# Optimization experiments

Measured on AMD Instinct MI355X. Metric: run time of the kernel, lower is better.

## Reference

```python
import jax, jax.numpy as jnp
import numpy as np
from jax.ops import segment_sum, segment_max

N_NODES = 100000
N_EDGES = 1600000
IN_CH = 128
HIDDEN = 128
OUT_CH = 64
HEADS1 = 8


def _lin_params(key, din, dout, scale):
    kw, kb = jax.random.split(key)
    W = jax.random.normal(kw, (din, dout), jnp.float32) * scale
    b = jax.random.normal(kb, (dout,), jnp.float32) * 0.01
    return W, b


def setup_inputs() -> dict:
    key = jax.random.key(0)
    ks = jax.random.split(key, 10)
    x = jax.random.normal(ks[0], (N_NODES, IN_CH), jnp.float32)
    edge_index = jax.random.randint(ks[1], (2, N_EDGES), 0, N_NODES, jnp.int32)
    s1 = 1.0 / np.sqrt(IN_CH)
    Wq1, bq1 = _lin_params(ks[2], IN_CH, HIDDEN, s1)
    Wk1, bk1 = _lin_params(ks[3], IN_CH, HIDDEN, s1)
    Wv1, bv1 = _lin_params(ks[4], IN_CH, HIDDEN, s1)
    Ws1, bs1 = _lin_params(ks[5], IN_CH, HIDDEN, s1)
    s2 = 1.0 / np.sqrt(HIDDEN)
    Wq2, bq2 = _lin_params(ks[6], HIDDEN, OUT_CH, s2)
    Wk2, bk2 = _lin_params(ks[7], HIDDEN, OUT_CH, s2)
    Wv2, bv2 = _lin_params(ks[8], HIDDEN, OUT_CH, s2)
    Ws2, bs2 = _lin_params(ks[9], HIDDEN, OUT_CH, s2)
    return dict(x=x, edge_index=edge_index,
                Wq1=Wq1, bq1=bq1, Wk1=Wk1, bk1=bk1, Wv1=Wv1, bv1=bv1, Ws1=Ws1, bs1=bs1,
                Wq2=Wq2, bq2=bq2, Wk2=Wk2, bk2=bk2, Wv2=Wv2, bv2=bv2, Ws2=Ws2, bs2=bs2)


def transformer_conv(x, src, dst, Wq, bq, Wk, bk, Wv, bv, Ws, bs, heads, concat):
    # x: [N, Din]; src/dst: [E]; per-head dim C = Dout_total // heads
    N = x.shape[0]
    C = Wq.shape[1] // heads
    q = (x @ Wq + bq).reshape(N, heads, C)
    k = (x @ Wk + bk).reshape(N, heads, C)
    v = (x @ Wv + bv).reshape(N, heads, C)
    # edge-wise gather + dot-product attention logits: [E, H]
    alpha = jnp.einsum('ehc,ehc->eh', q[dst], k[src]) / np.sqrt(C)
    # softmax over incoming edges of each dst node (stable via segment max)
    m = segment_max(alpha, dst, num_segments=N)  # [N, H]
    ex = jnp.exp(alpha - jax.lax.stop_gradient(m)[dst])
    denom = segment_sum(ex, dst, num_segments=N)  # [N, H]
    alpha_n = ex / denom[dst]  # [E, H]
    out = segment_sum(v[src] * alpha_n[:, :, None], dst, num_segments=N)  # [N, H, C]
    skip = x @ Ws + bs  # root weight (PyG root_weight=True)
    if concat:
        out = out.reshape(N, heads * C) + skip
    else:
        out = out.mean(axis=1) + skip
    return out


def reference(x, edge_index,
              Wq1, bq1, Wk1, bk1, Wv1, bv1, Ws1, bs1,
              Wq2, bq2, Wk2, bk2, Wv2, bv2, Ws2, bs2):
    src, dst = edge_index[0], edge_index[1]
    h = transformer_conv(x, src, dst, Wq1, bq1, Wk1, bk1, Wv1, bv1, Ws1, bs1,
                         heads=HEADS1, concat=True)
    h = jax.nn.relu(h)  # dropout is identity in eval mode
    out = transformer_conv(h, src, dst, Wq2, bq2, Wk2, bk2, Wv2, bv2, Ws2, bs2,
                           heads=1, concat=False)
    return out
```

## Files before the change

### kernel.cpp

```cpp
#include <hip/hip_runtime.h>
#include <math.h>

#define NN 100000
#define NE 1600000
#define NB 391
#define BKSH 8
#define EPB 6250
#define CSTAGE 5120
#define NDEG 64
#define DTOT (NDEG * NB)

typedef __attribute__((ext_vector_type(8))) short bf16x8;
typedef __attribute__((ext_vector_type(4))) float f32x4;

__device__ __forceinline__ unsigned short f2bf(float x) {
  unsigned int u = __float_as_uint(x);
  u += 0x7fffu + ((u >> 16) & 1u);
  return (unsigned short)(u >> 16);
}
__device__ __forceinline__ float bf2f(unsigned short b) {
  return __uint_as_float(((unsigned int)b) << 16);
}
__device__ __forceinline__ void unpack8(uint4 u, float* f) {
  f[0] = __uint_as_float(u.x << 16); f[1] = __uint_as_float(u.x & 0xffff0000u);
  f[2] = __uint_as_float(u.y << 16); f[3] = __uint_as_float(u.y & 0xffff0000u);
  f[4] = __uint_as_float(u.z << 16); f[5] = __uint_as_float(u.z & 0xffff0000u);
  f[6] = __uint_as_float(u.w << 16); f[7] = __uint_as_float(u.w & 0xffff0000u);
}
__device__ __forceinline__ void split8(const float* f, bf16x8& h8, bf16x8& l8) {
  union { bf16x8 v; unsigned short s[8]; } H, L;
  #pragma unroll
  for (int j = 0; j < 8; ++j) {
    const unsigned short hh = f2bf(f[j]);
    H.s[j] = hh;
    L.s[j] = f2bf(f[j] - bf2f(hh));
  }
  h8 = H.v; l8 = L.v;
}
__device__ __forceinline__ void gl_lds16(const void* g, void* lds) {
  __builtin_amdgcn_global_load_lds(
      (const __attribute__((address_space(1))) unsigned int*)g,
      (__attribute__((address_space(3))) unsigned int*)lds, 16, 0, 0);
}

#define PIPE_WAIT16 asm volatile("s_waitcnt vmcnt(16)\n\ts_barrier" ::: "memory")
#define PIPE_WAIT0  asm volatile("s_waitcnt vmcnt(0)\n\ts_barrier" ::: "memory")
#define PIPE_BAR    asm volatile("s_barrier" ::: "memory")

__global__ __launch_bounds__(256)
void bktcnt_k(const int* __restrict__ dst, int* __restrict__ gcnt) {
  __shared__ int cnt[NB];
  for (int i = threadIdx.x; i < NB; i += 256) cnt[i] = 0;
  __syncthreads();
  const int e0 = blockIdx.x * EPB;
  for (int e = e0 + threadIdx.x; e < e0 + EPB; e += 256)
    atomicAdd(&cnt[dst[e] >> BKSH], 1);
  __syncthreads();
  for (int i = threadIdx.x; i < NB; i += 256)
    if (cnt[i]) atomicAdd(&gcnt[i], cnt[i]);
}

__global__ void bktscan_k(const int* __restrict__ gcnt, int* __restrict__ base,
                          int* __restrict__ cursor) {
  __shared__ int sh[512];
  const int t = threadIdx.x;
  const int v = (t < NB) ? gcnt[t] : 0;
  sh[t] = v;
  __syncthreads();
  #pragma unroll
  for (int off = 1; off < 512; off <<= 1) {
    int nv = (t >= off) ? sh[t - off] : 0;
    __syncthreads();
    sh[t] += nv;
    __syncthreads();
  }
  const int excl = sh[t] - v;
  if (t < NB) { base[t] = excl; cursor[t] = excl; }
  if (t == NB - 1) base[NB] = excl + v;
}

__global__ __launch_bounds__(256)
void bktscat_k(const int* __restrict__ src, const int* __restrict__ dst,
               int* __restrict__ cursor, unsigned int* __restrict__ pairs) {
  __shared__ int cnt[NB];
  __shared__ int bbase[NB];
  for (int i = threadIdx.x; i < NB; i += 256) cnt[i] = 0;
  __syncthreads();
  const int e0 = blockIdx.x * EPB;
  for (int e = e0 + threadIdx.x; e < e0 + EPB; e += 256)
    atomicAdd(&cnt[dst[e] >> BKSH], 1);
  __syncthreads();
  for (int i = threadIdx.x; i < NB; i += 256) {
    bbase[i] = cnt[i] ? atomicAdd(&cursor[i], cnt[i]) : 0;
    cnt[i] = 0;
  }
  __syncthreads();
  for (int e = e0 + threadIdx.x; e < e0 + EPB; e += 256) {
    const int d = dst[e];
    const int b = d >> BKSH;
    const int loc = atomicAdd(&cnt[b], 1);
    pairs[bbase[b] + loc] = ((unsigned)src[e] << BKSH) | (unsigned)(d & 255);
  }
}

__global__ __launch_bounds__(256)
void bktcsr_k(const unsigned int* __restrict__ pairs, const int* __restrict__ base,
              int* __restrict__ rowp, int* __restrict__ cidx) {
  __shared__ int cnt[256];
  __shared__ int sums[256];
  __shared__ int stage[CSTAGE];
  const int b = blockIdx.x, t = threadIdx.x;
  const int p0 = base[b], p1 = base[b + 1], bs = p1 - p0;
  const int n0 = b << BKSH;
  const int nloc = (NN - n0 < 256) ? (NN - n0) : 256;
  cnt[t] = 0;
  __syncthreads();
  for (int i = p0 + t; i < p1; i += 256)
    atomicAdd(&cnt[pairs[i] & 255], 1);
  __syncthreads();
  const int v = cnt[t];
  sums[t] = v;
  __syncthreads();
  #pragma unroll
  for (int off = 1; off < 256; off <<= 1) {
    int nv = (t >= off) ? sums[t - off] : 0;
    __syncthreads();
    sums[t] += nv;
    __syncthreads();
  }
  const int myexcl = sums[t] - v;
  if (t < nloc) rowp[n0 + t] = p0 + myexcl;
  if (b == 0 && t == 0) rowp[NN] = base[NB];
  __syncthreads();
  cnt[t] = myexcl;
  __syncthreads();
  if (bs <= CSTAGE) {
    for (int i = p0 + t; i < p1; i += 256) {
      const unsigned pk = pairs[i];
      const int loc = atomicAdd(&cnt[pk & 255], 1);
      stage[loc] = (int)(pk >> BKSH);
    }
    __syncthreads();
    for (int i = t; i < bs; i += 256) cidx[p0 + i] = stage[i];
  } else {
    for (int i = p0 + t; i < p1; i += 256) {
      const unsigned pk = pairs[i];
      const int loc = atomicAdd(&cnt[pk & 255], 1);
      cidx[p0 + loc] = (int)(pk >> BKSH);
    }
  }
}

__global__ __launch_bounds__(256)
void dcnt_k(const int* __restrict__ rowp, int* __restrict__ gdcnt) {
  __shared__ int h[NDEG];
  const int t = threadIdx.x, b = blockIdx.x;
  if (t < NDEG) h[t] = 0;
  __syncthreads();
  const int n = b * 256 + t;
  if (n < NN) {
    int d = rowp[n + 1] - rowp[n];
    if (d > NDEG - 1) d = NDEG - 1;
    atomicAdd(&h[d], 1);
  }
  __syncthreads();
  if (t < NDEG) gdcnt[t * NB + b] = h[t];
}

__global__ __launch_bounds__(1024)
void dscan2_k(int* __restrict__ g) {
  __shared__ int part[1024];
  const int t = threadIdx.x;
  constexpr int PER = (DTOT + 1023) / 1024;
  int vals[PER];
  const int base = t * PER;
  int sum = 0;
  #pragma unroll
  for (int i = 0; i < PER; ++i) {
    const int idx = base + i;
    const int v = (idx < DTOT) ? g[idx] : 0;
    vals[i] = sum;
    sum += v;
  }
  part[t] = sum;
  __syncthreads();
  #pragma unroll
  for (int off = 1; off < 1024; off <<= 1) {
    int nv = (t >= off) ? part[t - off] : 0;
    __syncthreads();
    part[t] += nv;
    __syncthreads();
  }
  const int excl = part[t] - sum;
  #pragma unroll
  for (int i = 0; i < PER; ++i) {
    const int idx = base + i;
    if (idx < DTOT) g[idx] = excl + vals[i];
  }
}

__global__ __launch_bounds__(256)
void dperm2_k(const int* __restrict__ rowp, const int* __restrict__ gdcnt,
              int* __restrict__ perm) {
  __shared__ int lcur[NDEG];
  const int t = threadIdx.x, b = blockIdx.x;
  if (t < NDEG) lcur[t] = 0;
  __syncthreads();
  const int n = b * 256 + t;
  if (n < NN) {
    int d = rowp[n + 1] - rowp[n];
    if (d > NDEG - 1) d = NDEG - 1;
    const int r = atomicAdd(&lcur[d], 1);
    perm[gdcnt[d * NB + b] + r] = n;
  }
}

struct WConv { const float* src; unsigned short* hi; unsigned short* lo; int dout; };
struct WConv8 { WConv m[8]; };

__global__ void wconv_k(WConv8 a) {
  const WConv w = a.m[blockIdx.x];
  const int n = 128 * w.dout;
  for (int i = threadIdx.x; i < n; i += blockDim.x) {
    const int c = i >> 7, kk = i & 127;
    const float x = w.src[(size_t)kk * w.dout + c];
    const unsigned short h = f2bf(x);
    w.hi[i] = h;
    w.lo[i] = f2bf(x - bf2f(h));
  }
}

struct GMat { const unsigned short* wh; const unsigned short* wl;
              const float* bias; float* outf; unsigned short* outb; };
struct GArgs { GMat m[4]; };

template <int DOUT, bool PRESPLIT>
__global__ __launch_bounds__(256, 3)
void gemm4_mfma(const float* __restrict__ X,
                const unsigned short* __restrict__ Xh,
                const unsigned short* __restrict__ Xl,
                int nrows, GArgs ga) {
  constexpr int NCG = DOUT / 64;
  constexpr int NS = 4 * NCG * 2;
  __shared__ __align__(16) unsigned short Bs[2][8192];
  const int t = threadIdx.x;
  const int w = t >> 6, l = t & 63;
  const int lr = l & 15, lg = l >> 4;
  const int row0 = blockIdx.x * 128;

  bf16x8 ah[2][4], al[2][4];
  #pragma unroll
  for (int rf = 0; rf < 2; ++rf) {
    const int r = row0 + w * 32 + rf * 16 + lr;
    const bool ok = r < nrows;
    if constexpr (!PRESPLIT) {
      const float* xp = &X[(size_t)r * 128];
      #pragma unroll
      for (int ks = 0; ks < 4; ++ks) {
        float f[8];
        if (ok) {
          *(float4*)&f[0] = *(const float4*)&xp[ks * 32 + lg * 8];
          *(float4*)&f[4] = *(const float4*)&xp[ks * 32 + lg * 8 + 4];
        } else {
          #pragma unroll
          for (int j = 0; j < 8; ++j) f[j] = 0.f;
        }
        split8(f, ah[rf][ks], al[rf][ks]);
      }
    } else {
      #pragma unroll
      for (int ks = 0; ks < 4; ++ks) {
        if (ok) {
          ah[rf][ks] = *(const bf16x8*)&Xh[(size_t)r * 128 + ks * 32 + lg * 8];
          al[rf][ks] = *(const bf16x8*)&Xl[(size_t)r * 128 + ks * 32 + lg * 8];
        } else {
          union { bf16x8 v; unsigned short s[8]; } z;
          #pragma unroll
          for (int j = 0; j < 8; ++j) z.s[j] = 0;
          ah[rf][ks] = z.v; al[rf][ks] = z.v;
        }
      }
    }
  }

  auto stage = [&](int buf, int s) {
    const int m = s / (NCG * 2);
    const int rem = s - m * (NCG * 2);
    const int cg = rem >> 1, pl = rem & 1;
    const char* gb = (const char*)((pl ? ga.m[m].wl : ga.m[m].wh) + cg * 64 * 128);
    char* lb = (char*)&Bs[buf][0];
    #pragma unroll
    for (int i = 0; i < 4; ++i) {
      const int seg = (w * 4 + i) << 10;
      const int o = seg + l * 16;
      const int osw = o ^ (((o >> 8) & 7) << 4);
      gl_lds16(gb + osw, lb + seg);
    }
  };

  f32x4 acc[4][2];
  stage(0, 0);
  int cur = 0;
  const int sw = (lr & 7) << 4;
  for (int s = 0; s < NS; ++s) {
    if (s + 1 < NS) {
      stage(cur ^ 1, s + 1);
      PIPE_WAIT16;
    } else {
      PIPE_WAIT0;
    }
    const int m = s / (NCG * 2);
    const int rem = s - m * (NCG * 2);
    const int cg = rem >> 1, pl = rem & 1;
    const char* lbase = (const char*)&Bs[cur][0];
    if (pl == 0) {
      #pragma unroll
      for (int nf = 0; nf < 4; ++nf) {
        const char* lp = lbase + nf * 4096 + lr * 256;
        bf16x8 bq[4];
        #pragma unroll
        for (int ks = 0; ks < 4; ++ks)
          bq[ks] = *(const bf16x8*)(lp + (((ks * 64 + lg * 16) ^ sw)));
        f32x4 a0 = {0.f, 0.f, 0.f, 0.f}, a1 = a0;
        #pragma unroll
        for (int ks = 0; ks < 4; ++ks) {
          a0 = __builtin_amdgcn_mfma_f32_16x16x32_bf16(ah[0][ks], bq[ks], a0, 0, 0, 0);
          a1 = __builtin_amdgcn_mfma_f32_16x16x32_bf16(ah[1][ks], bq[ks], a1, 0, 0, 0);
        }
        #pragma unroll
        for (int ks = 0; ks < 4; ++ks) {
          a0 = __builtin_amdgcn_mfma_f32_16x16x32_bf16(al[0][ks], bq[ks], a0, 0, 0, 0);
          a1 = __builtin_amdgcn_mfma_f32_16x16x32_bf16(al[1][ks], bq[ks], a1, 0, 0, 0);
        }
        acc[nf][0] = a0; acc[nf][1] = a1;
      }
    } else {
      const GMat gm = ga.m[m];
      #pragma unroll
      for (int nf = 0; nf < 4; ++nf) {
        const char* lp = lbase + nf * 4096 + lr * 256;
        bf16x8 bq[4];
        #pragma unroll
        for (int ks = 0; ks < 4; ++ks)
          bq[ks] = *(const bf16x8*)(lp + (((ks * 64 + lg * 16) ^ sw)));
        f32x4 a0 = acc[nf][0], a1 = acc[nf][1];
        #pragma unroll
        for (int ks = 0; ks < 4; ++ks) {
          a0 = __builtin_amdgcn_mfma_f32_16x16x32_bf16(ah[0][ks], bq[ks], a0, 0, 0, 0);
          a1 = __builtin_amdgcn_mfma_f32_16x16x32_bf16(ah[1][ks], bq[ks], a1, 0, 0, 0);
        }
        const int col = cg * 64 + nf * 16 + lr;
        const float bb = gm.bias[col];
        #pragma unroll
        for (int j = 0; j < 4; ++j) {
          const int r0 = row0 + w * 32 + lg * 4 + j;
          const int r1 = r0 + 16;
          if (gm.outb) {
            if (r0 < nrows) gm.outb[(size_t)r0 * DOUT + col] = f2bf(a0[j] + bb);
            if (r1 < nrows) gm.outb[(size_t)r1 * DOUT + col] = f2bf(a1[j] + bb);
          } else {
            if (r0 < nrows) gm.outf[(size_t)r0 * DOUT + col] = a0[j] + bb;
            if (r1 < nrows) gm.outf[(size_t)r1 * DOUT + col] = a1[j] + bb;
          }
        }
      }
    }
    if (s + 1 < NS) PIPE_BAR;
    cur ^= 1;
  }
}

__global__ __launch_bounds__(256)
void attn1_k(const unsigned short* __restrict__ q, const unsigned short* __restrict__ k,
             const unsigned short* __restrict__ v, const float* __restrict__ skip,
             const int* __restrict__ rowp, const int* __restrict__ cidx,
             const int* __restrict__ perm,
             unsigned short* __restrict__ hhi, unsigned short* __restrict__ hlo) {
  const int idx = blockIdx.x * 32 + (threadIdx.x >> 3);
  if (idx >= NN) return;
  const int node = perm[idx];
  const int cb = (threadIdx.x & 7) * 16;
  float qv[16];
  {
    uint4 q0 = *(const uint4*)&q[(size_t)node * 128 + cb];
    uint4 q1 = *(const uint4*)&q[(size_t)node * 128 + cb + 8];
    unpack8(q0, qv); unpack8(q1, qv + 8);
    #pragma unroll
    for (int c = 0; c < 16; ++c) qv[c] *= 0.25f;
  }
  float s = 0.f, acc[16];
  #pragma unroll
  for (int c = 0; c < 16; ++c) acc[c] = 0.f;
  const int e0 = rowp[node], e1 = rowp[node + 1];
  int e = e0;
  for (; e + 3 < e1; e += 4) {
    int sidx[4];
    #pragma unroll
    for (int j = 0; j < 4; ++j) sidx[j] = cidx[e + j];
    uint4 K[4][2], V[4][2];
    #pragma unroll
    for (int j = 0; j < 4; ++j) {
      const size_t o = (size_t)sidx[j] * 128 + cb;
      K[j][0] = *(const uint4*)&k[o];
      K[j][1] = *(const uint4*)&k[o + 8];
      V[j][0] = *(const uint4*)&v[o];
      V[j][1] = *(const uint4*)&v[o + 8];
    }
    float pr[4];
    #pragma unroll
    for (int j = 0; j < 4; ++j) {
      float kv[16];
      unpack8(K[j][0], kv); unpack8(K[j][1], kv + 8);
      float d = 0.f;
      #pragma unroll
      for (int c = 0; c < 16; ++c) d = fmaf(qv[c], kv[c], d);
      pr[j] = __expf(d);
      s += pr[j];
    }
    #pragma unroll
    for (int j = 0; j < 4; ++j) {
      float vv[16];
      unpack8(V[j][0], vv); unpack8(V[j][1], vv + 8);
      #pragma unroll
      for (int c = 0; c < 16; ++c) acc[c] = fmaf(pr[j], vv[c], acc[c]);
    }
  }
  for (; e < e1; ++e) {
    const int sa = cidx[e];
    uint4 k0 = *(const uint4*)&k[(size_t)sa * 128 + cb];
    uint4 k1 = *(const uint4*)&k[(size_t)sa * 128 + cb + 8];
    uint4 v0 = *(const uint4*)&v[(size_t)sa * 128 + cb];
    uint4 v1 = *(const uint4*)&v[(size_t)sa * 128 + cb + 8];
    float kv[16]; unpack8(k0, kv); unpack8(k1, kv + 8);
    float d = 0.f;
    #pragma unroll
    for (int c = 0; c < 16; ++c) d = fmaf(qv[c], kv[c], d);
    const float p = __expf(d);
    s += p;
    float vv[16]; unpack8(v0, vv); unpack8(v1, vv + 8);
    #pragma unroll
    for (int c = 0; c < 16; ++c) acc[c] = fmaf(p, vv[c], acc[c]);
  }
  const float inv = (e1 > e0) ? 1.f / s : 0.f;
  float sk[16];
  {
    const float* sp = &skip[(size_t)node * 128 + cb];
    *(float4*)&sk[0]  = *(const float4*)&sp[0];
    *(float4*)&sk[4]  = *(const float4*)&sp[4];
    *(float4*)&sk[8]  = *(const float4*)&sp[8];
    *(float4*)&sk[12] = *(const float4*)&sp[12];
  }
  unsigned int hw[8], lw[8];
  #pragma unroll
  for (int c2 = 0; c2 < 8; ++c2) {
    const float oa = fmaxf(fmaf(acc[2 * c2], inv, sk[2 * c2]), 0.f);
    const float ob = fmaxf(fmaf(acc[2 * c2 + 1], inv, sk[2 * c2 + 1]), 0.f);
    const unsigned short ha = f2bf(oa), hb = f2bf(ob);
    hw[c2] = (unsigned)ha | ((unsigned)hb << 16);
    lw[c2] = (unsigned)f2bf(oa - bf2f(ha)) | ((unsigned)f2bf(ob - bf2f(hb)) << 16);
  }
  uint4* HH = (uint4*)&hhi[(size_t)node * 128 + cb];
  uint4* LL = (uint4*)&hlo[(size_t)node * 128 + cb];
  HH[0] = make_uint4(hw[0], hw[1], hw[2], hw[3]);
  HH[1] = make_uint4(hw[4], hw[5], hw[6], hw[7]);
  LL[0] = make_uint4(lw[0], lw[1], lw[2], lw[3]);
  LL[1] = make_uint4(lw[4], lw[5], lw[6], lw[7]);
}

__global__ __launch_bounds__(256)
void attn2_k(const unsigned short* __restrict__ q, const unsigned short* __restrict__ k,
             const unsigned short* __restrict__ v, const float* __restrict__ skip,
             const int* __restrict__ rowp, const int* __restrict__ cidx,
             const int* __restrict__ perm, float* __restrict__ out) {
  const int idx = blockIdx.x * 32 + (threadIdx.x >> 3);
  if (idx >= NN) return;
  const int node = perm[idx];
  const int cb = (threadIdx.x & 7) * 8;
  float qv[8];
  {
    uint4 q0 = *(const uint4*)&q[(size_t)node * 64 + cb];
    unpack8(q0, qv);
    #pragma unroll
    for (int c = 0; c < 8; ++c) qv[c] *= 0.125f;
  }
  float s = 0.f, acc[8];
  #pragma unroll
  for (int c = 0; c < 8; ++c) acc[c] = 0.f;
  const int e0 = rowp[node], e1 = rowp[node + 1];
  int e = e0;
  for (; e + 3 < e1; e += 4) {
    int sidx[4];
    #pragma unroll
    for (int j = 0; j < 4; ++j) sidx[j] = cidx[e + j];
    uint4 K[4], V[4];
    #pragma unroll
    for (int j = 0; j < 4; ++j) {
      const size_t o = (size_t)sidx[j] * 64 + cb;
      K[j] = *(const uint4*)&k[o];
      V[j] = *(const uint4*)&v[o];
    }
    float dd[4];
    #pragma unroll
    for (int j = 0; j < 4; ++j) {
      float kv[8]; unpack8(K[j], kv);
      float d = 0.f;
      #pragma unroll
      for (int c = 0; c < 8; ++c) d = fmaf(qv[c], kv[c], d);
      dd[j] = d;
    }
    #pragma unroll
    for (int j = 0; j < 4; ++j) {
      dd[j] += __shfl_xor(dd[j], 1);
      dd[j] += __shfl_xor(dd[j], 2);
      dd[j] += __shfl_xor(dd[j], 4);
    }
    #pragma unroll
    for (int j = 0; j < 4; ++j) {
      const float p = __expf(dd[j]);
      s += p;
      float vv[8]; unpack8(V[j], vv);
      #pragma unroll
      for (int c = 0; c < 8; ++c) acc[c] = fmaf(p, vv[c], acc[c]);
    }
  }
  for (; e < e1; ++e) {
    const int sa = cidx[e];
    uint4 kk = *(const uint4*)&k[(size_t)sa * 64 + cb];
    uint4 vv4 = *(const uint4*)&v[(size_t)sa * 64 + cb];
    float kv[8]; unpack8(kk, kv);
    float d = 0.f;
    #pragma unroll
    for (int c = 0; c < 8; ++c) d = fmaf(qv[c], kv[c], d);
    d += __shfl_xor(d, 1);
    d += __shfl_xor(d, 2);
    d += __shfl_xor(d, 4);
    const float p = __expf(d);
    s += p;
    float vv[8]; unpack8(vv4, vv);
    #pragma unroll
    for (int c = 0; c < 8; ++c) acc[c] = fmaf(p, vv[c], acc[c]);
  }
  const float inv = (e1 > e0) ? 1.f / s : 0.f;
  const float* sp = &skip[(size_t)node * 64 + cb];
  float4 o0, o1;
  o0.x = fmaf(acc[0], inv, sp[0]); o0.y = fmaf(acc[1], inv, sp[1]);
  o0.z = fmaf(acc[2], inv, sp[2]); o0.w = fmaf(acc[3], inv, sp[3]);
  o1.x = fmaf(acc[4], inv, sp[4]); o1.y = fmaf(acc[5], inv, sp[5]);
  o1.z = fmaf(acc[6], inv, sp[6]); o1.w = fmaf(acc[7], inv, sp[7]);
  *(float4*)&out[(size_t)node * 64 + cb] = o0;
  *(float4*)&out[(size_t)node * 64 + cb + 4] = o1;
}

extern "C" void kernel_launch(void* const* d_in, const int* in_sizes, int n_in,
                              void* d_out, int out_size, void* d_ws, size_t ws_size,
                              hipStream_t stream) {
  const float* x = (const float*)d_in[0];
  const int* ei = (const int*)d_in[1];
  const int* esrc = ei;
  const int* edst = ei + NE;
  const float* Wf[8] = {(const float*)d_in[2],  (const float*)d_in[4],
                        (const float*)d_in[6],  (const float*)d_in[8],
                        (const float*)d_in[10], (const float*)d_in[12],
                        (const float*)d_in[14], (const float*)d_in[16]};
  const float* Bf[8] = {(const float*)d_in[3],  (const float*)d_in[5],
                        (const float*)d_in[7],  (const float*)d_in[9],
                        (const float*)d_in[11], (const float*)d_in[13],
                        (const float*)d_in[15], (const float*)d_in[17]};
  float* out = (float*)d_out;

  char* p = (char*)d_ws;
  auto alloc = [&](size_t b) { char* r = p; p += (b + 255) & ~(size_t)255; return r; };
  unsigned short* q1 = (unsigned short*)alloc((size_t)NN * 128 * 2);
  unsigned short* k1 = (unsigned short*)alloc((size_t)NN * 128 * 2);
  unsigned short* v1 = (unsigned short*)alloc((size_t)NN * 128 * 2);
  float*          sk1 = (float*)alloc((size_t)NN * 128 * 4);
  unsigned short* hh = (unsigned short*)alloc((size_t)NN * 128 * 2);
  unsigned short* hl = (unsigned short*)alloc((size_t)NN * 128 * 2);
  unsigned short* q2 = (unsigned short*)alloc((size_t)NN * 64 * 2);
  unsigned short* k2 = (unsigned short*)alloc((size_t)NN * 64 * 2);
  unsigned short* v2 = (unsigned short*)alloc((size_t)NN * 64 * 2);
  float*          sk2 = (float*)alloc((size_t)NN * 64 * 4);
  unsigned short* wh[8];
  unsigned short* wl[8];
  for (int i = 0; i < 8; ++i) {
    const int dout = (i < 4) ? 128 : 64;
    wh[i] = (unsigned short*)alloc((size_t)128 * dout * 2);
    wl[i] = (unsigned short*)alloc((size_t)128 * dout * 2);
  }
  int* rowp = (int*)alloc((size_t)(NN + 1) * 4);
  int* cidx = (int*)alloc((size_t)NE * 4);
  int* gcnt = (int*)alloc((size_t)NB * 4);
  int* base = (int*)alloc((size_t)(NB + 1) * 4);
  int* cursor = (int*)alloc((size_t)NB * 4);
  int* gdcnt = (int*)alloc((size_t)DTOT * 4);
  int* perm = (int*)alloc((size_t)NN * 4);
  unsigned int* pairs = (unsigned int*)hh;

  WConv8 wc;
  for (int i = 0; i < 8; ++i) wc.m[i] = {Wf[i], wh[i], wl[i], (i < 4) ? 128 : 64};
  wconv_k<<<8, 1024, 0, stream>>>(wc);

  hipMemsetAsync(gcnt, 0, NB * sizeof(int), stream);
  bktcnt_k<<<256, 256, 0, stream>>>(edst, gcnt);
  bktscan_k<<<1, 512, 0, stream>>>(gcnt, base, cursor);
  bktscat_k<<<256, 256, 0, stream>>>(esrc, edst, cursor, pairs);
  bktcsr_k<<<NB, 256, 0, stream>>>(pairs, base, rowp, cidx);

  dcnt_k<<<NB, 256, 0, stream>>>(rowp, gdcnt);
  dscan2_k<<<1, 1024, 0, stream>>>(gdcnt);
  dperm2_k<<<NB, 256, 0, stream>>>(rowp, gdcnt, perm);

  GArgs g1;
  g1.m[0] = {wh[0], wl[0], Bf[0], nullptr, q1};
  g1.m[1] = {wh[1], wl[1], Bf[1], nullptr, k1};
  g1.m[2] = {wh[2], wl[2], Bf[2], nullptr, v1};
  g1.m[3] = {wh[3], wl[3], Bf[3], sk1, nullptr};
  gemm4_mfma<128, false><<<(NN + 127) / 128, 256, 0, stream>>>(x, nullptr, nullptr, NN, g1);
  attn1_k<<<(NN + 31) / 32, 256, 0, stream>>>(q1, k1, v1, sk1, rowp, cidx, perm, hh, hl);

  GArgs g2;
  g2.m[0] = {wh[4], wl[4], Bf[4], nullptr, q2};
  g2.m[1] = {wh[5], wl[5], Bf[5], nullptr, k2};
  g2.m[2] = {wh[6], wl[6], Bf[6], nullptr, v2};
  g2.m[3] = {wh[7], wl[7], Bf[7], sk2, nullptr};
  gemm4_mfma<64, true><<<(NN + 127) / 128, 256, 0, stream>>>(nullptr, hh, hl, NN, g2);
  attn2_k<<<(NN + 31) / 32, 256, 0, stream>>>(q2, k2, v2, sk2, rowp, cidx, perm, out);
}
```

Measured before the change: 474.9 us.

## Pad node buffers, drop GEMM bounds checks, preload bias, retune waitcnt pipeline

Node-indexed intermediate buffers are padded to a multiple of 128 rows, so the GEMM kernels can drop per-row bounds checks on loads and stores. Bias values are preloaded into registers, and the stage loop is fully unrolled with finer vmcnt waits that account for the extra outstanding loads. The degree-sorted node permutation is reversed so high-degree nodes are scheduled first in the attention kernels, aiming at better tail load balance. The changes cost more register pressure in the GEMM and some extra memory, and they rely on exact vmcnt counts being correct.

```diff
diff --git a/kernel.cpp b/kernel.cpp
--- a/kernel.cpp
+++ b/kernel.cpp
@@ -2,6 +2,7 @@
 #include <math.h>
 
 #define NN 100000
+#define NPAD 100096
 #define NE 1600000
 #define NB 391
 #define BKSH 8
@@ -43,9 +44,11 @@
       (__attribute__((address_space(3))) unsigned int*)lds, 16, 0, 0);
 }
 
-#define PIPE_WAIT16 asm volatile("s_waitcnt vmcnt(16)\n\ts_barrier" ::: "memory")
+#define PIPE_WAIT4  asm volatile("s_waitcnt vmcnt(4)\n\ts_barrier" ::: "memory")
+#define PIPE_WAIT36 asm volatile("s_waitcnt vmcnt(36)\n\ts_barrier" ::: "memory")
 #define PIPE_WAIT0  asm volatile("s_waitcnt vmcnt(0)\n\ts_barrier" ::: "memory")
 #define PIPE_BAR    asm volatile("s_barrier" ::: "memory")
+#define PIPE_FENCE  asm volatile("" ::: "memory")
 
 __global__ __launch_bounds__(256)
 void bktcnt_k(const int* __restrict__ dst, int* __restrict__ gcnt) {
@@ -211,7 +214,7 @@
     int d = rowp[n + 1] - rowp[n];
     if (d > NDEG - 1) d = NDEG - 1;
     const int r = atomicAdd(&lcur[d], 1);
-    perm[gdcnt[d * NB + b] + r] = n;
+    perm[NN - 1 - (gdcnt[d * NB + b] + r)] = n;
   }
 }
 
@@ -248,12 +251,21 @@
   const int lr = l & 15, lg = l >> 4;
   const int row0 = blockIdx.x * 128;
 
+  float bias_r[4][NCG][4];
+  #pragma unroll
+  for (int m = 0; m < 4; ++m)
+    #pragma unroll
+    for (int cg = 0; cg < NCG; ++cg)
+      #pragma unroll
+      for (int nf = 0; nf < 4; ++nf)
+        bias_r[m][cg][nf] = ga.m[m].bias[cg * 64 + nf * 16 + lr];
+
   bf16x8 ah[2][4], al[2][4];
   #pragma unroll
   for (int rf = 0; rf < 2; ++rf) {
     const int r = row0 + w * 32 + rf * 16 + lr;
-    const bool ok = r < nrows;
     if constexpr (!PRESPLIT) {
+      const bool ok = r < nrows;
       const float* xp = &X[(size_t)r * 128];
       #pragma unroll
       for (int ks = 0; ks < 4; ++ks) {
@@ -270,18 +282,12 @@
     } else {
       #pragma unroll
       for (int ks = 0; ks < 4; ++ks) {
-        if (ok) {
-          ah[rf][ks] = *(const bf16x8*)&Xh[(size_t)r * 128 + ks * 32 + lg * 8];
-          al[rf][ks] = *(const bf16x8*)&Xl[(size_t)r * 128 + ks * 32 + lg * 8];
-        } else {
-          union { bf16x8 v; unsigned short s[8]; } z;
-          #pragma unroll
-          for (int j = 0; j < 8; ++j) z.s[j] = 0;
-          ah[rf][ks] = z.v; al[rf][ks] = z.v;
-        }
+        ah[rf][ks] = *(const bf16x8*)&Xh[(size_t)r * 128 + ks * 32 + lg * 8];
+        al[rf][ks] = *(const bf16x8*)&Xl[(size_t)r * 128 + ks * 32 + lg * 8];
       }
     }
   }
+  PIPE_FENCE;
 
   auto stage = [&](int buf, int s) {
     const int m = s / (NCG * 2);
@@ -302,13 +308,12 @@
   stage(0, 0);
   int cur = 0;
   const int sw = (lr & 7) << 4;
+  #pragma unroll
   for (int s = 0; s < NS; ++s) {
-    if (s + 1 < NS) {
-      stage(cur ^ 1, s + 1);
-      PIPE_WAIT16;
-    } else {
-      PIPE_WAIT0;
-    }
+    if (s + 1 < NS) stage(cur ^ 1, s + 1);
+    if (s == NS - 1)                { PIPE_WAIT0; }
+    else if (s >= 2 && !(s & 1))    { PIPE_WAIT36; }
+    else                            { PIPE_WAIT4;  }
     const int m = s / (NCG * 2);
     const int rem = s - m * (NCG * 2);
     const int cg = rem >> 1, pl = rem & 1;
@@ -350,17 +355,17 @@
           a1 = __builtin_amdgcn_mfma_f32_16x16x32_bf16(ah[1][ks], bq[ks], a1, 0, 0, 0);
         }
         const int col = cg * 64 + nf * 16 + lr;
-        const float bb = gm.bias[col];
+        const float bb = bias_r[m][cg][nf];
         #pragma unroll
         for (int j = 0; j < 4; ++j) {
           const int r0 = row0 + w * 32 + lg * 4 + j;
           const int r1 = r0 + 16;
           if (gm.outb) {
-            if (r0 < nrows) gm.outb[(size_t)r0 * DOUT + col] = f2bf(a0[j] + bb);
-            if (r1 < nrows) gm.outb[(size_t)r1 * DOUT + col] = f2bf(a1[j] + bb);
+            gm.outb[(size_t)r0 * DOUT + col] = f2bf(a0[j] + bb);
+            gm.outb[(size_t)r1 * DOUT + col] = f2bf(a1[j] + bb);
           } else {
-            if (r0 < nrows) gm.outf[(size_t)r0 * DOUT + col] = a0[j] + bb;
-            if (r1 < nrows) gm.outf[(size_t)r1 * DOUT + col] = a1[j] + bb;
+            gm.outf[(size_t)r0 * DOUT + col] = a0[j] + bb;
+            gm.outf[(size_t)r1 * DOUT + col] = a1[j] + bb;
           }
         }
       }
@@ -570,16 +575,16 @@
 
   char* p = (char*)d_ws;
   auto alloc = [&](size_t b) { char* r = p; p += (b + 255) & ~(size_t)255; return r; };
-  unsigned short* q1 = (unsigned short*)alloc((size_t)NN * 128 * 2);
-  unsigned short* k1 = (unsigned short*)alloc((size_t)NN * 128 * 2);
-  unsigned short* v1 = (unsigned short*)alloc((size_t)NN * 128 * 2);
-  float*          sk1 = (float*)alloc((size_t)NN * 128 * 4);
-  unsigned short* hh = (unsigned short*)alloc((size_t)NN * 128 * 2);
-  unsigned short* hl = (unsigned short*)alloc((size_t)NN * 128 * 2);
-  unsigned short* q2 = (unsigned short*)alloc((size_t)NN * 64 * 2);
-  unsigned short* k2 = (unsigned short*)alloc((size_t)NN * 64 * 2);
-  unsigned short* v2 = (unsigned short*)alloc((size_t)NN * 64 * 2);
-  float*          sk2 = (float*)alloc((size_t)NN * 64 * 4);
+  unsigned short* q1 = (unsigned short*)alloc((size_t)NPAD * 128 * 2);
+  unsigned short* k1 = (unsigned short*)alloc((size_t)NPAD * 128 * 2);
+  unsigned short* v1 = (unsigned short*)alloc((size_t)NPAD * 128 * 2);
+  float*          sk1 = (float*)alloc((size_t)NPAD * 128 * 4);
+  unsigned short* hh = (unsigned short*)alloc((size_t)NPAD * 128 * 2);
+  unsigned short* hl = (unsigned short*)alloc((size_t)NPAD * 128 * 2);
+  unsigned short* q2 = (unsigned short*)alloc((size_t)NPAD * 64 * 2);
+  unsigned short* k2 = (unsigned short*)alloc((size_t)NPAD * 64 * 2);
+  unsigned short* v2 = (unsigned short*)alloc((size_t)NPAD * 64 * 2);
+  float*          sk2 = (float*)alloc((size_t)NPAD * 64 * 4);
   unsigned short* wh[8];
   unsigned short* wl[8];
   for (int i = 0; i < 8; ++i) {
@@ -615,7 +620,7 @@
   g1.m[1] = {wh[1], wl[1], Bf[1], nullptr, k1};
   g1.m[2] = {wh[2], wl[2], Bf[2], nullptr, v1};
   g1.m[3] = {wh[3], wl[3], Bf[3], sk1, nullptr};
-  gemm4_mfma<128, false><<<(NN + 127) / 128, 256, 0, stream>>>(x, nullptr, nullptr, NN, g1);
+  gemm4_mfma<128, false><<<NPAD / 128, 256, 0, stream>>>(x, nullptr, nullptr, NN, g1);
   attn1_k<<<(NN + 31) / 32, 256, 0, stream>>>(q1, k1, v1, sk1, rowp, cidx, perm, hh, hl);
 
   GArgs g2;
@@ -623,6 +628,6 @@
   g2.m[1] = {wh[5], wl[5], Bf[5], nullptr, k2};
   g2.m[2] = {wh[6], wl[6], Bf[6], nullptr, v2};
   g2.m[3] = {wh[7], wl[7], Bf[7], sk2, nullptr};
-  gemm4_mfma<64, true><<<(NN + 127) / 128, 256, 0, stream>>>(nullptr, hh, hl, NN, g2);
+  gemm4_mfma<64, true><<<NPAD / 128, 256, 0, stream>>>(nullptr, hh, hl, NN, g2);
   attn2_k<<<(NN + 31) / 32, 256, 0, stream>>>(q2, k2, v2, sk2, rowp, cidx, perm, out);
 }
```

Result: faster. 433.7 us (-8.7%).
